# Performance work log

Hardware: AMD Instinct MI355X
Metric: run time of the kernel (lower is better)

Reference implementation:

```python
import jax, jax.numpy as jnp
import numpy as np

B = 1024        # probe batch
Q = 65536       # queue_size (number of identities in momentum queue)
D = 512         # feat_dim
MARGIN = 0.4
SCALE = 32.0
HARD_NEG = 10   # min(max(int(Q*0.0002), 3), 10)


def setup_inputs() -> dict:
    key = jax.random.key(0)
    k1, k2, k3, k4 = jax.random.split(key, 4)
    p = jax.random.normal(k1, (B, D), dtype=jnp.float32)
    p = p / jnp.linalg.norm(p, axis=1, keepdims=True)
    queue = jax.random.uniform(k2, (2, Q, D), dtype=jnp.float32)
    queue = queue / jnp.linalg.norm(queue, axis=2, keepdims=True)  # F.normalize(queue, dim=2)
    label = jax.random.randint(k3, (B,), 0, Q)
    label = jnp.where(jnp.arange(B) % 4 == 0, -1, label)
    # binary mask buffer marking queue slots whose second copy is active
    mask = (jax.random.uniform(k4, (Q, 1)) < 0.1).astype(jnp.float32)
    return {"p": p, "queue": queue, "mask": mask, "label": label}


def _add_margin_am(cos_theta, label):
    # cos_theta: [B, Q], label: [B] with -1 marking outliers
    pos_mask = label != -1                                  # [B]
    safe_label = jnp.where(pos_mask, label, 0)
    onehot = jax.nn.one_hot(safe_label, cos_theta.shape[1], dtype=cos_theta.dtype)
    # AM-softmax: subtract margin at the ground-truth logit, then scale + CE
    logits = (cos_theta - MARGIN * onehot) * SCALE          # [B, Q]
    log_z = jax.nn.logsumexp(logits, axis=1)                # [B]
    gt = jnp.take_along_axis(cos_theta, safe_label[:, None], axis=1)[:, 0]
    ce = log_z - (gt - MARGIN) * SCALE                      # per-row cross entropy
    n_pos = jnp.sum(pos_mask)
    cls_loss = jnp.where(
        n_pos > 0,
        jnp.sum(jnp.where(pos_mask, ce, 0.0)) / jnp.maximum(n_pos, 1),
        0.0,
    )
    # hard-negative mining over outlier rows: top-k (replaces torch argsort+gather)
    top_vals, _ = jax.lax.top_k(cos_theta, HARD_NEG)        # [B, HARD_NEG]
    hard = jnp.clip(top_vals, 0.0)
    neg_per_row = jnp.mean(hard, axis=1)                    # [B]
    n_neg = jnp.sum(~pos_mask)
    neg_loss = jnp.where(
        n_neg > 0,
        jnp.sum(jnp.where(~pos_mask, neg_per_row, 0.0)) / jnp.maximum(n_neg, 1),
        0.0,
    )
    return cls_loss + neg_loss


def reference(p, queue, mask, label):
    # cos_theta1 = F.linear(p, queue[0])
    cos1 = jnp.einsum('bd,qd->bq', p, queue[0])
    # weight = mask * queue[1] + (1 - mask) * queue[0]  (computed under no_grad in torch)
    weight = mask * queue[1] + (1.0 - mask) * queue[0]
    cos2 = jnp.einsum('bd,qd->bq', p, weight)
    loss = _add_margin_am(cos1, label) + _add_margin_am(cos2, label)
    return loss
```

## Files before the change

kernel.cpp:

```cpp
#include <hip/hip_runtime.h>
#include <stdint.h>

#define B_ 1024
#define Q_ 65536
#define D_ 512
#define MT 128
#define NT 128
#define BK 64
#define NSPLIT 64
#define NCHUNK (Q_ / NSPLIT)
#define NTILES (NCHUNK / NT)
#define KITERS (D_ / BK)

#define WS_ACC  0
#define WS_LSE  1024
#define WS_TOPK (WS_LSE + 2 * B_ * NSPLIT * 2 * 4)
#define WS_PBF  (8u * 1024u * 1024u)
#define WS_QBF  (16u * 1024u * 1024u)

#define SA_OFF 0
#define SB0_OFF 16384
#define SB1_OFF 32768
#define EPI_STRIDE 264
#define EPI1_OFF 33792
#define SMEM_BYTES 67584

typedef __attribute__((ext_vector_type(8))) short short8;
typedef __attribute__((ext_vector_type(4))) short short4v;
typedef __attribute__((ext_vector_type(4))) float f32x4;

__device__ __forceinline__ unsigned short f2bf(float x) {
  union { float f; uint32_t u; } v; v.f = x;
  uint32_t r = v.u + 0x7fffu + ((v.u >> 16) & 1u);
  return (unsigned short)(r >> 16);
}

__device__ __forceinline__ float bf2f(short u) {
  union { uint32_t i; float f; } v;
  v.i = ((uint32_t)(unsigned short)u) << 16;
  return v.f;
}

__device__ __forceinline__ void async16(void* lds, const void* g) {
  void* gg = (void*)g;
  __builtin_amdgcn_global_load_lds(
      (__attribute__((address_space(1))) unsigned int*)gg,
      (__attribute__((address_space(3))) unsigned int*)lds,
      16, 0, 0);
}

__device__ __forceinline__ void lse_bf_row(const unsigned char* rowp,
                                           float& M, float& Z) {
  float tmax = -1e30f;
#pragma unroll
  for (int c = 0; c < 32; ++c) {
    short4v v = *(const short4v*)(rowp + c * 8);
    tmax = fmaxf(tmax, fmaxf(fmaxf(bf2f(v.x), bf2f(v.y)),
                             fmaxf(bf2f(v.z), bf2f(v.w))));
  }
  float Mn = fmaxf(M, tmax * 32.0f);
  float fac = __expf(M - Mn);
  float s = 0.0f;
#pragma unroll
  for (int c = 0; c < 32; ++c) {
    short4v v = *(const short4v*)(rowp + c * 8);
    s += __expf(fmaf(bf2f(v.x), 32.0f, -Mn));
    s += __expf(fmaf(bf2f(v.y), 32.0f, -Mn));
    s += __expf(fmaf(bf2f(v.z), 32.0f, -Mn));
    s += __expf(fmaf(bf2f(v.w), 32.0f, -Mn));
  }
  Z = fmaf(Z, fac, s);
  M = Mn;
}

__device__ __forceinline__ void tkins(float v,
    float& t0, float& t1, float& t2, float& t3, float& t4,
    float& t5, float& t6, float& t7, float& t8, float& t9) {
  if (v > t9) {
    t9 = (v > t8) ? t8 : v;
    t8 = (v > t8) ? ((v > t7) ? t7 : v) : t8;
    t7 = (v > t7) ? ((v > t6) ? t6 : v) : t7;
    t6 = (v > t6) ? ((v > t5) ? t5 : v) : t6;
    t5 = (v > t5) ? ((v > t4) ? t4 : v) : t5;
    t4 = (v > t4) ? ((v > t3) ? t3 : v) : t4;
    t3 = (v > t3) ? ((v > t2) ? t2 : v) : t3;
    t2 = (v > t2) ? ((v > t1) ? t1 : v) : t2;
    t1 = (v > t1) ? ((v > t0) ? t0 : v) : t1;
    t0 = (v > t0) ? v : t0;
  }
}

#define TK10(v, base) tkins((v), rs[(base)+0], rs[(base)+1], rs[(base)+2], rs[(base)+3], \
    rs[(base)+4], rs[(base)+5], rs[(base)+6], rs[(base)+7], rs[(base)+8], rs[(base)+9])

__global__ void cvt_bf16_kernel(const float* __restrict__ src,
                                unsigned short* __restrict__ dst, int n8) {
  int i = blockIdx.x * blockDim.x + threadIdx.x;
  int stride = gridDim.x * blockDim.x;
  for (; i < n8; i += stride) {
    const float4* s = (const float4*)src + (size_t)2 * i;
    float4 a = s[0], b = s[1];
    short8 o;
    o[0] = (short)f2bf(a.x); o[1] = (short)f2bf(a.y);
    o[2] = (short)f2bf(a.z); o[3] = (short)f2bf(a.w);
    o[4] = (short)f2bf(b.x); o[5] = (short)f2bf(b.y);
    o[6] = (short)f2bf(b.z); o[7] = (short)f2bf(b.w);
    *(short8*)(dst + (size_t)i * 8) = o;
  }
}

__global__ __launch_bounds__(256, 2) void fused_gemm_partial(
    const unsigned short* __restrict__ pbf, const unsigned short* __restrict__ qbf,
    const float* __restrict__ maskp, const int* __restrict__ label,
    char* __restrict__ ws) {
  __shared__ __align__(16) unsigned char smem[SMEM_BYTES];
  __shared__ float maskbuf[NT];
  __shared__ int olist[MT];
  __shared__ int sh_ocount;

  float* tlbuf = (float*)smem;

  const int tid = threadIdx.x;
  const int mblk = blockIdx.x;
  const int split = blockIdx.y;
  const int lane = tid & 63;
  const int wv = tid >> 6;
  const int wr = wv >> 1;
  const int wc = wv & 1;
  const int lr = lane & 15;
  const int lg = lane >> 4;

  if (tid == 0) sh_ocount = 0;
  __syncthreads();
  if (tid < MT) {
    if (label[mblk * MT + tid] == -1) {
      int k = atomicAdd(&sh_ocount, 1);
      olist[k] = tid;
    }
  }
  __syncthreads();
  const int noc = sh_ocount;
  int rowloc = -1;
  int sub = 0;
  if (tid >= 128) {
    int task = (tid - 128) >> 2;
    sub = (tid - 128) & 3;
    if (task < noc) rowloc = olist[task];
  }

  const int srow = lane >> 3;
  const int sc16 = (lane & 7) ^ srow;
  const size_t g_lane_off = (size_t)srow * D_ + sc16 * 8;

  float rs[20];
#pragma unroll
  for (int i = 0; i < 20; ++i) rs[i] = -1e30f;
  if (tid < MT) { rs[1] = 0.0f; rs[3] = 0.0f; }

  for (int nt = 0; nt < NTILES; ++nt) {
    const int nbase = split * NCHUNK + nt * NT;
    if (tid < NT) maskbuf[tid] = maskp[nbase + tid];

    f32x4 acc0[4][4], acc1[4][4];
#pragma unroll
    for (int i = 0; i < 4; ++i)
#pragma unroll
      for (int j = 0; j < 4; ++j) {
        f32x4 z = {0.0f, 0.0f, 0.0f, 0.0f};
        acc0[i][j] = z;
        acc1[i][j] = z;
      }

    for (int kk = 0; kk < KITERS; ++kk) {
      const size_t kcol = (size_t)kk * BK;
#pragma unroll
      for (int t = 0; t < 4; ++t) {
        const int slot = wv * 4 + t;
        const size_t rbase = (size_t)slot * 8;
        async16(smem + SA_OFF + slot * 1024,
                pbf + ((size_t)mblk * MT + rbase) * D_ + kcol + g_lane_off);
        async16(smem + SB0_OFF + slot * 1024,
                qbf + ((size_t)nbase + rbase) * D_ + kcol + g_lane_off);
        async16(smem + SB1_OFF + slot * 1024,
                qbf + ((size_t)Q_ + nbase + rbase) * D_ + kcol + g_lane_off);
      }
      __syncthreads();

#pragma unroll
      for (int s = 0; s < 2; ++s) {
        const int xs = ((s * 4 + lg) ^ (lr & 7)) * 16;
        short8 af[4], bf0[4], bf1[4];
#pragma unroll
        for (int i = 0; i < 4; ++i)
          af[i] = *(const short8*)(smem + SA_OFF + (wr * 64 + i * 16 + lr) * 128 + xs);
#pragma unroll
        for (int j = 0; j < 4; ++j) {
          bf0[j] = *(const short8*)(smem + SB0_OFF + (wc * 64 + j * 16 + lr) * 128 + xs);
          bf1[j] = *(const short8*)(smem + SB1_OFF + (wc * 64 + j * 16 + lr) * 128 + xs);
        }
#pragma unroll
        for (int i = 0; i < 4; ++i)
#pragma unroll
          for (int j = 0; j < 4; ++j) {
            acc0[i][j] = __builtin_amdgcn_mfma_f32_16x16x32_bf16(af[i], bf0[j], acc0[i][j], 0, 0, 0);
            acc1[i][j] = __builtin_amdgcn_mfma_f32_16x16x32_bf16(af[i], bf1[j], acc1[i][j], 0, 0, 0);
          }
      }
      __syncthreads();
    }

    float mcol[4];
#pragma unroll
    for (int j = 0; j < 4; ++j) mcol[j] = maskbuf[wc * 64 + j * 16 + lr];
#pragma unroll
    for (int i = 0; i < 4; ++i)
#pragma unroll
      for (int j = 0; j < 4; ++j)
#pragma unroll
        for (int k = 0; k < 4; ++k) {
          const int r = wr * 64 + i * 16 + lg * 4 + k;
          const int c = wc * 64 + j * 16 + lr;
          float g0 = acc0[i][j][k], g1 = acc1[i][j][k];
          *(unsigned short*)(smem + r * EPI_STRIDE + c * 2) = f2bf(g0);
          *(unsigned short*)(smem + EPI1_OFF + r * EPI_STRIDE + c * 2) =
              f2bf(fmaf(mcol[j], g1 - g0, g0));
        }
    __syncthreads();

    if (tid < MT) {
      lse_bf_row(smem + tid * EPI_STRIDE, rs[0], rs[1]);
      lse_bf_row(smem + EPI1_OFF + tid * EPI_STRIDE, rs[2], rs[3]);
    } else if (rowloc >= 0) {
      const unsigned char* b0 = smem + rowloc * EPI_STRIDE + sub * 64;
#pragma unroll
      for (int c = 0; c < 8; ++c) {
        short4v v = *(const short4v*)(b0 + c * 8);
        TK10(bf2f(v.x), 0); TK10(bf2f(v.y), 0);
        TK10(bf2f(v.z), 0); TK10(bf2f(v.w), 0);
      }
      const unsigned char* b1 = b0 + EPI1_OFF;
#pragma unroll
      for (int c = 0; c < 8; ++c) {
        short4v v = *(const short4v*)(b1 + c * 8);
        TK10(bf2f(v.x), 10); TK10(bf2f(v.y), 10);
        TK10(bf2f(v.z), 10); TK10(bf2f(v.w), 10);
      }
    }
    __syncthreads();
  }

  if (tid < MT) {
    int grow = mblk * MT + tid;
    float2* lseo = (float2*)(ws + WS_LSE);
    lseo[((size_t)0 * B_ + grow) * NSPLIT + split] = make_float2(rs[0], rs[1]);
    lseo[((size_t)1 * B_ + grow) * NSPLIT + split] = make_float2(rs[2], rs[3]);
  }
  if (tid >= 128) {
    float* dst = &tlbuf[(tid - 128) * 20];
#pragma unroll
    for (int i = 0; i < 20; ++i) dst[i] = rs[i];
  }
  __syncthreads();
  if (tid < 64) {
    int l = tid & 1, o = tid >> 1;
    if (o < noc) {
      float m0 = -1e30f, m1 = -1e30f, m2 = -1e30f, m3 = -1e30f, m4 = -1e30f;
      float m5 = -1e30f, m6 = -1e30f, m7 = -1e30f, m8 = -1e30f, m9 = -1e30f;
#pragma unroll
      for (int s = 0; s < 4; ++s)
#pragma unroll
        for (int i = 0; i < 10; ++i)
          tkins(tlbuf[(o * 4 + s) * 20 + l * 10 + i], m0, m1, m2, m3, m4, m5, m6, m7, m8, m9);
      int grow = mblk * MT + olist[o];
      float* dst = (float*)(ws + WS_TOPK) + ((size_t)(l * B_ + grow) * NSPLIT + (size_t)split) * 10;
      dst[0] = m0; dst[1] = m1; dst[2] = m2; dst[3] = m3; dst[4] = m4;
      dst[5] = m5; dst[6] = m6; dst[7] = m7; dst[8] = m8; dst[9] = m9;
    }
  }
}

__global__ void finalize_rows(
    const float* __restrict__ p, const float* __restrict__ queue,
    const float* __restrict__ maskp, const int* __restrict__ label,
    char* __restrict__ ws) {
  const int row = blockIdx.x;
  const int l = threadIdx.x >> 6;
  const int lane = threadIdx.x & 63;
  const int lab = label[row];
  float* wsf = (float*)ws;
  int* wsi = (int*)ws;

  if (lab != -1) {
    const float2* lsep = (const float2*)(ws + WS_LSE);
    float2 mz = lsep[((size_t)l * B_ + row) * NSPLIT + lane];
    float M = mz.x;
    float Mx = M;
#pragma unroll
    for (int o = 1; o < 64; o <<= 1) Mx = fmaxf(Mx, __shfl_xor(Mx, o, 64));
    float z = mz.y * __expf(M - Mx);
#pragma unroll
    for (int o = 1; o < 64; o <<= 1) z += __shfl_xor(z, o, 64);

    const float* prow = p + (size_t)row * D_;
    const float* q0r = queue + (size_t)lab * D_;
    const float* q1r = queue + ((size_t)Q_ + (size_t)lab) * D_;
    int c = lane * 8;
    float4 a0 = *(const float4*)(prow + c);
    float4 a1 = *(const float4*)(prow + c + 4);
    float4 b0 = *(const float4*)(q0r + c);
    float4 b1 = *(const float4*)(q0r + c + 4);
    float d0 = a0.x * b0.x + a0.y * b0.y + a0.z * b0.z + a0.w * b0.w
             + a1.x * b1.x + a1.y * b1.y + a1.z * b1.z + a1.w * b1.w;
    float d1 = 0.0f;
    if (l == 1) {
      float4 c0 = *(const float4*)(q1r + c);
      float4 c1 = *(const float4*)(q1r + c + 4);
      d1 = a0.x * c0.x + a0.y * c0.y + a0.z * c0.z + a0.w * c0.w
         + a1.x * c1.x + a1.y * c1.y + a1.z * c1.z + a1.w * c1.w;
    }
#pragma unroll
    for (int o = 1; o < 64; o <<= 1) {
      d0 += __shfl_xor(d0, o, 64);
      d1 += __shfl_xor(d1, o, 64);
    }
    float gt;
    if (l == 0) gt = d0;
    else { float m = maskp[lab]; gt = fmaf(m, d1 - d0, d0); }

    if (lane == 0) {
      float t1 = __expf(fmaf(gt, 32.0f, -Mx));
      float t2 = __expf(fmaf(gt - 0.4f, 32.0f, -Mx));
      float Zc = z - t1 + t2;
      float ce = Mx + __logf(Zc) - (gt - 0.4f) * 32.0f;
      atomicAdd(&wsf[0], ce);
      if (l == 0) atomicAdd(&wsi[2], 1);
    }
  } else {
    const float* tp = (const float*)(ws + WS_TOPK) +
                      ((size_t)(l * B_ + row) * NSPLIT + (size_t)lane) * 10;
    float t0 = tp[0], t1 = tp[1], t2 = tp[2], t3 = tp[3], t4 = tp[4];
    float t5 = tp[5], t6 = tp[6], t7 = tp[7], t8 = tp[8], t9 = tp[9];
    float ssum = 0.0f;
#pragma unroll
    for (int r10 = 0; r10 < 10; ++r10) {
      float v = t0;
      int idx = lane;
#pragma unroll
      for (int o = 1; o < 64; o <<= 1) {
        float ov = __shfl_xor(v, o, 64);
        int oi = __shfl_xor(idx, o, 64);
        bool take = (ov > v) || (ov == v && oi < idx);
        v = take ? ov : v;
        idx = take ? oi : idx;
      }
      ssum += fmaxf(v, 0.0f);
      if (idx == lane) {
        t0 = t1; t1 = t2; t2 = t3; t3 = t4; t4 = t5;
        t5 = t6; t6 = t7; t7 = t8; t8 = t9; t9 = -1e30f;
      }
    }
    if (lane == 0) {
      atomicAdd(&wsf[1], ssum * 0.1f);
      if (l == 0) atomicAdd(&wsi[3], 1);
    }
  }
}

__global__ void finalize_scalar(const char* __restrict__ ws, float* __restrict__ out) {
  const float* wsf = (const float*)ws;
  const int* wsi = (const int*)ws;
  float loss = 0.0f;
  if (wsi[2] > 0) loss += wsf[0] / (float)wsi[2];
  if (wsi[3] > 0) loss += wsf[1] / (float)wsi[3];
  out[0] = loss;
}

extern "C" void kernel_launch(void* const* d_in, const int* in_sizes, int n_in,
                              void* d_out, int out_size, void* d_ws, size_t ws_size,
                              hipStream_t stream) {
  const float* p     = (const float*)d_in[0];
  const float* queue = (const float*)d_in[1];
  const float* maskp = (const float*)d_in[2];
  const int*   label = (const int*)d_in[3];
  float* out = (float*)d_out;
  char* ws = (char*)d_ws;

  unsigned short* pbf = (unsigned short*)(ws + WS_PBF);
  unsigned short* qbf = (unsigned short*)(ws + WS_QBF);

  hipMemsetAsync(ws, 0, 16, stream);

  cvt_bf16_kernel<<<4096, 256, 0, stream>>>(queue, qbf, (2 * Q_ * D_) / 8);
  cvt_bf16_kernel<<<256, 256, 0, stream>>>(p, pbf, (B_ * D_) / 8);

  dim3 g1(B_ / MT, NSPLIT);
  fused_gemm_partial<<<g1, 256, 0, stream>>>(pbf, qbf, maskp, label, ws);
  finalize_rows<<<B_, 128, 0, stream>>>(p, queue, maskp, label, ws);
  finalize_scalar<<<1, 1, 0, stream>>>(ws, out);
}
```

Before: 638.9 us.

## Precompute mixed weight matrix in conversion pass and split GEMM per logit set

The conversion kernel now blends queue[0] and queue[1] by the mask into a separate bf16 weight matrix, and reads queue[1] only for rows whose mask is set. Each GEMM block therefore computes one logit set, against either queue0 or the blended weight. This drops the per-element mask blend in the epilogue, halves the accumulator registers and LDS per block, and raises occupancy to three blocks per CU. The split count doubles and the grid is reordered, which increases the partial results the finalize kernel must merge. Numerics change slightly because the blend now happens in fp32 before the bf16 rounding.

```diff
diff --git a/kernel.cpp b/kernel.cpp
--- a/kernel.cpp
+++ b/kernel.cpp
@@ -7,7 +7,7 @@
 #define MT 128
 #define NT 128
 #define BK 64
-#define NSPLIT 64
+#define NSPLIT 128
 #define NCHUNK (Q_ / NSPLIT)
 #define NTILES (NCHUNK / NT)
 #define KITERS (D_ / BK)
@@ -15,15 +15,14 @@
 #define WS_ACC  0
 #define WS_LSE  1024
 #define WS_TOPK (WS_LSE + 2 * B_ * NSPLIT * 2 * 4)
-#define WS_PBF  (8u * 1024u * 1024u)
-#define WS_QBF  (16u * 1024u * 1024u)
+#define WS_PBF  (13u * 1024u * 1024u)
+#define WS_QBF0 (14u * 1024u * 1024u)
+#define WS_WBF  (78u * 1024u * 1024u)
 
 #define SA_OFF 0
-#define SB0_OFF 16384
-#define SB1_OFF 32768
+#define SB_OFF 16384
 #define EPI_STRIDE 264
-#define EPI1_OFF 33792
-#define SMEM_BYTES 67584
+#define SMEM_BYTES 33792
 
 typedef __attribute__((ext_vector_type(8))) short short8;
 typedef __attribute__((ext_vector_type(4))) short short4v;
@@ -90,8 +89,39 @@
   }
 }
 
-#define TK10(v, base) tkins((v), rs[(base)+0], rs[(base)+1], rs[(base)+2], rs[(base)+3], \
-    rs[(base)+4], rs[(base)+5], rs[(base)+6], rs[(base)+7], rs[(base)+8], rs[(base)+9])
+#define TK10(v) tkins((v), rs[0], rs[1], rs[2], rs[3], rs[4], rs[5], rs[6], rs[7], rs[8], rs[9])
+
+__global__ void cvt_queue_kernel(const float* __restrict__ q,
+                                 const float* __restrict__ mask,
+                                 unsigned short* __restrict__ qbf0,
+                                 unsigned short* __restrict__ wbf) {
+  const int row = blockIdx.x * 4 + (threadIdx.x >> 6);
+  const int lane = threadIdx.x & 63;
+  const float* q0r = q + (size_t)row * D_ + lane * 8;
+  float4 a = ((const float4*)q0r)[0];
+  float4 b = ((const float4*)q0r)[1];
+  short8 o;
+  o[0] = (short)f2bf(a.x); o[1] = (short)f2bf(a.y);
+  o[2] = (short)f2bf(a.z); o[3] = (short)f2bf(a.w);
+  o[4] = (short)f2bf(b.x); o[5] = (short)f2bf(b.y);
+  o[6] = (short)f2bf(b.z); o[7] = (short)f2bf(b.w);
+  *(short8*)(qbf0 + (size_t)row * D_ + lane * 8) = o;
+  float m = mask[row];
+  if (m != 0.0f) {
+    const float* q1r = q0r + (size_t)Q_ * D_;
+    float4 c = ((const float4*)q1r)[0];
+    float4 d = ((const float4*)q1r)[1];
+    a.x = fmaf(m, c.x - a.x, a.x); a.y = fmaf(m, c.y - a.y, a.y);
+    a.z = fmaf(m, c.z - a.z, a.z); a.w = fmaf(m, c.w - a.w, a.w);
+    b.x = fmaf(m, d.x - b.x, b.x); b.y = fmaf(m, d.y - b.y, b.y);
+    b.z = fmaf(m, d.z - b.z, b.z); b.w = fmaf(m, d.w - b.w, b.w);
+    o[0] = (short)f2bf(a.x); o[1] = (short)f2bf(a.y);
+    o[2] = (short)f2bf(a.z); o[3] = (short)f2bf(a.w);
+    o[4] = (short)f2bf(b.x); o[5] = (short)f2bf(b.y);
+    o[6] = (short)f2bf(b.z); o[7] = (short)f2bf(b.w);
+  }
+  *(short8*)(wbf + (size_t)row * D_ + lane * 8) = o;
+}
 
 __global__ void cvt_bf16_kernel(const float* __restrict__ src,
                                 unsigned short* __restrict__ dst, int n8) {
@@ -109,20 +139,22 @@
   }
 }
 
-__global__ __launch_bounds__(256, 2) void fused_gemm_partial(
-    const unsigned short* __restrict__ pbf, const unsigned short* __restrict__ qbf,
-    const float* __restrict__ maskp, const int* __restrict__ label,
+__global__ __launch_bounds__(256, 3) void fused_gemm_partial(
+    const unsigned short* __restrict__ pbf,
+    const unsigned short* __restrict__ qbf0,
+    const unsigned short* __restrict__ wbf,
+    const int* __restrict__ label,
     char* __restrict__ ws) {
   __shared__ __align__(16) unsigned char smem[SMEM_BYTES];
-  __shared__ float maskbuf[NT];
   __shared__ int olist[MT];
   __shared__ int sh_ocount;
-
   float* tlbuf = (float*)smem;
 
   const int tid = threadIdx.x;
-  const int mblk = blockIdx.x;
-  const int split = blockIdx.y;
+  const int split = blockIdx.x;
+  const int mblk = blockIdx.y >> 1;
+  const int which = blockIdx.y & 1;
+  const unsigned short* bsrc = which ? wbf : qbf0;
   const int lane = tid & 63;
   const int wv = tid >> 6;
   const int wr = wv >> 1;
@@ -152,23 +184,21 @@
   const int sc16 = (lane & 7) ^ srow;
   const size_t g_lane_off = (size_t)srow * D_ + sc16 * 8;
 
-  float rs[20];
-#pragma unroll
-  for (int i = 0; i < 20; ++i) rs[i] = -1e30f;
-  if (tid < MT) { rs[1] = 0.0f; rs[3] = 0.0f; }
+  float rs[10];
+#pragma unroll
+  for (int i = 0; i < 10; ++i) rs[i] = -1e30f;
+  if (tid < MT) rs[1] = 0.0f;
 
   for (int nt = 0; nt < NTILES; ++nt) {
     const int nbase = split * NCHUNK + nt * NT;
-    if (tid < NT) maskbuf[tid] = maskp[nbase + tid];
-
-    f32x4 acc0[4][4], acc1[4][4];
+
+    f32x4 acc[4][4];
 #pragma unroll
     for (int i = 0; i < 4; ++i)
 #pragma unroll
       for (int j = 0; j < 4; ++j) {
         f32x4 z = {0.0f, 0.0f, 0.0f, 0.0f};
-        acc0[i][j] = z;
-        acc1[i][j] = z;
+        acc[i][j] = z;
       }
 
     for (int kk = 0; kk < KITERS; ++kk) {
@@ -179,39 +209,30 @@
         const size_t rbase = (size_t)slot * 8;
         async16(smem + SA_OFF + slot * 1024,
                 pbf + ((size_t)mblk * MT + rbase) * D_ + kcol + g_lane_off);
-        async16(smem + SB0_OFF + slot * 1024,
-                qbf + ((size_t)nbase + rbase) * D_ + kcol + g_lane_off);
-        async16(smem + SB1_OFF + slot * 1024,
-                qbf + ((size_t)Q_ + nbase + rbase) * D_ + kcol + g_lane_off);
+        async16(smem + SB_OFF + slot * 1024,
+                bsrc + ((size_t)nbase + rbase) * D_ + kcol + g_lane_off);
       }
       __syncthreads();
 
 #pragma unroll
       for (int s = 0; s < 2; ++s) {
         const int xs = ((s * 4 + lg) ^ (lr & 7)) * 16;
-        short8 af[4], bf0[4], bf1[4];
+        short8 af[4], bf[4];
 #pragma unroll
         for (int i = 0; i < 4; ++i)
           af[i] = *(const short8*)(smem + SA_OFF + (wr * 64 + i * 16 + lr) * 128 + xs);
 #pragma unroll
-        for (int j = 0; j < 4; ++j) {
-          bf0[j] = *(const short8*)(smem + SB0_OFF + (wc * 64 + j * 16 + lr) * 128 + xs);
-          bf1[j] = *(const short8*)(smem + SB1_OFF + (wc * 64 + j * 16 + lr) * 128 + xs);
-        }
+        for (int j = 0; j < 4; ++j)
+          bf[j] = *(const short8*)(smem + SB_OFF + (wc * 64 + j * 16 + lr) * 128 + xs);
 #pragma unroll
         for (int i = 0; i < 4; ++i)
 #pragma unroll
-          for (int j = 0; j < 4; ++j) {
-            acc0[i][j] = __builtin_amdgcn_mfma_f32_16x16x32_bf16(af[i], bf0[j], acc0[i][j], 0, 0, 0);
-            acc1[i][j] = __builtin_amdgcn_mfma_f32_16x16x32_bf16(af[i], bf1[j], acc1[i][j], 0, 0, 0);
-          }
+          for (int j = 0; j < 4; ++j)
+            acc[i][j] = __builtin_amdgcn_mfma_f32_16x16x32_bf16(af[i], bf[j], acc[i][j], 0, 0, 0);
       }
       __syncthreads();
     }
 
-    float mcol[4];
-#pragma unroll
-    for (int j = 0; j < 4; ++j) mcol[j] = maskbuf[wc * 64 + j * 16 + lr];
 #pragma unroll
     for (int i = 0; i < 4; ++i)
 #pragma unroll
@@ -220,30 +241,17 @@
         for (int k = 0; k < 4; ++k) {
           const int r = wr * 64 + i * 16 + lg * 4 + k;
           const int c = wc * 64 + j * 16 + lr;
-          float g0 = acc0[i][j][k], g1 = acc1[i][j][k];
-          *(unsigned short*)(smem + r * EPI_STRIDE + c * 2) = f2bf(g0);
-          *(unsigned short*)(smem + EPI1_OFF + r * EPI_STRIDE + c * 2) =
-              f2bf(fmaf(mcol[j], g1 - g0, g0));
+          *(unsigned short*)(smem + r * EPI_STRIDE + c * 2) = f2bf(acc[i][j][k]);
         }
     __syncthreads();
-
     if (tid < MT) {
       lse_bf_row(smem + tid * EPI_STRIDE, rs[0], rs[1]);
-      lse_bf_row(smem + EPI1_OFF + tid * EPI_STRIDE, rs[2], rs[3]);
     } else if (rowloc >= 0) {
       const unsigned char* b0 = smem + rowloc * EPI_STRIDE + sub * 64;
 #pragma unroll
       for (int c = 0; c < 8; ++c) {
         short4v v = *(const short4v*)(b0 + c * 8);
-        TK10(bf2f(v.x), 0); TK10(bf2f(v.y), 0);
-        TK10(bf2f(v.z), 0); TK10(bf2f(v.w), 0);
-      }
-      const unsigned char* b1 = b0 + EPI1_OFF;
-#pragma unroll
-      for (int c = 0; c < 8; ++c) {
-        short4v v = *(const short4v*)(b1 + c * 8);
-        TK10(bf2f(v.x), 10); TK10(bf2f(v.y), 10);
-        TK10(bf2f(v.z), 10); TK10(bf2f(v.w), 10);
+        TK10(bf2f(v.x)); TK10(bf2f(v.y)); TK10(bf2f(v.z)); TK10(bf2f(v.w));
       }
     }
     __syncthreads();
@@ -252,30 +260,27 @@
   if (tid < MT) {
     int grow = mblk * MT + tid;
     float2* lseo = (float2*)(ws + WS_LSE);
-    lseo[((size_t)0 * B_ + grow) * NSPLIT + split] = make_float2(rs[0], rs[1]);
-    lseo[((size_t)1 * B_ + grow) * NSPLIT + split] = make_float2(rs[2], rs[3]);
+    lseo[((size_t)which * B_ + grow) * NSPLIT + split] = make_float2(rs[0], rs[1]);
   }
   if (tid >= 128) {
-    float* dst = &tlbuf[(tid - 128) * 20];
-#pragma unroll
-    for (int i = 0; i < 20; ++i) dst[i] = rs[i];
+    float* dst = &tlbuf[(tid - 128) * 10];
+#pragma unroll
+    for (int i = 0; i < 10; ++i) dst[i] = rs[i];
   }
   __syncthreads();
-  if (tid < 64) {
-    int l = tid & 1, o = tid >> 1;
-    if (o < noc) {
-      float m0 = -1e30f, m1 = -1e30f, m2 = -1e30f, m3 = -1e30f, m4 = -1e30f;
-      float m5 = -1e30f, m6 = -1e30f, m7 = -1e30f, m8 = -1e30f, m9 = -1e30f;
-#pragma unroll
-      for (int s = 0; s < 4; ++s)
-#pragma unroll
-        for (int i = 0; i < 10; ++i)
-          tkins(tlbuf[(o * 4 + s) * 20 + l * 10 + i], m0, m1, m2, m3, m4, m5, m6, m7, m8, m9);
-      int grow = mblk * MT + olist[o];
-      float* dst = (float*)(ws + WS_TOPK) + ((size_t)(l * B_ + grow) * NSPLIT + (size_t)split) * 10;
-      dst[0] = m0; dst[1] = m1; dst[2] = m2; dst[3] = m3; dst[4] = m4;
-      dst[5] = m5; dst[6] = m6; dst[7] = m7; dst[8] = m8; dst[9] = m9;
-    }
+  if (tid < 32 && tid < noc) {
+    float m0 = -1e30f, m1 = -1e30f, m2 = -1e30f, m3 = -1e30f, m4 = -1e30f;
+    float m5 = -1e30f, m6 = -1e30f, m7 = -1e30f, m8 = -1e30f, m9 = -1e30f;
+#pragma unroll
+    for (int s = 0; s < 4; ++s)
+#pragma unroll
+      for (int i = 0; i < 10; ++i)
+        tkins(tlbuf[(tid * 4 + s) * 10 + i], m0, m1, m2, m3, m4, m5, m6, m7, m8, m9);
+    int grow = mblk * MT + olist[tid];
+    float* dst = (float*)(ws + WS_TOPK) +
+                 ((size_t)which * B_ + grow) * NSPLIT * 10 + (size_t)split * 10;
+    dst[0] = m0; dst[1] = m1; dst[2] = m2; dst[3] = m3; dst[4] = m4;
+    dst[5] = m5; dst[6] = m6; dst[7] = m7; dst[8] = m8; dst[9] = m9;
   }
 }
 
@@ -291,13 +296,15 @@
   int* wsi = (int*)ws;
 
   if (lab != -1) {
-    const float2* lsep = (const float2*)(ws + WS_LSE);
-    float2 mz = lsep[((size_t)l * B_ + row) * NSPLIT + lane];
-    float M = mz.x;
+    const float2* lsep = (const float2*)(ws + WS_LSE) + ((size_t)l * B_ + row) * NSPLIT;
+    float2 a = lsep[lane];
+    float2 b = lsep[lane + 64];
+    float M = fmaxf(a.x, b.x);
+    float z = a.y * __expf(a.x - M) + b.y * __expf(b.x - M);
     float Mx = M;
 #pragma unroll
     for (int o = 1; o < 64; o <<= 1) Mx = fmaxf(Mx, __shfl_xor(Mx, o, 64));
-    float z = mz.y * __expf(M - Mx);
+    z *= __expf(M - Mx);
 #pragma unroll
     for (int o = 1; o < 64; o <<= 1) z += __shfl_xor(z, o, 64);
 
@@ -336,10 +343,14 @@
       if (l == 0) atomicAdd(&wsi[2], 1);
     }
   } else {
-    const float* tp = (const float*)(ws + WS_TOPK) +
-                      ((size_t)(l * B_ + row) * NSPLIT + (size_t)lane) * 10;
-    float t0 = tp[0], t1 = tp[1], t2 = tp[2], t3 = tp[3], t4 = tp[4];
-    float t5 = tp[5], t6 = tp[6], t7 = tp[7], t8 = tp[8], t9 = tp[9];
+    const float* tp = (const float*)(ws + WS_TOPK) + ((size_t)l * B_ + row) * NSPLIT * 10;
+    const float* pa = tp + (size_t)lane * 10;
+    const float* pb = tp + (size_t)(lane + 64) * 10;
+    float t0 = pa[0], t1 = pa[1], t2 = pa[2], t3 = pa[3], t4 = pa[4];
+    float t5 = pa[5], t6 = pa[6], t7 = pa[7], t8 = pa[8], t9 = pa[9];
+#pragma unroll
+    for (int i = 0; i < 10; ++i)
+      tkins(pb[i], t0, t1, t2, t3, t4, t5, t6, t7, t8, t9);
     float ssum = 0.0f;
 #pragma unroll
     for (int r10 = 0; r10 < 10; ++r10) {
@@ -385,16 +396,17 @@
   float* out = (float*)d_out;
   char* ws = (char*)d_ws;
 
-  unsigned short* pbf = (unsigned short*)(ws + WS_PBF);
-  unsigned short* qbf = (unsigned short*)(ws + WS_QBF);
+  unsigned short* pbf  = (unsigned short*)(ws + WS_PBF);
+  unsigned short* qbf0 = (unsigned short*)(ws + WS_QBF0);
+  unsigned short* wbf  = (unsigned short*)(ws + WS_WBF);
 
   hipMemsetAsync(ws, 0, 16, stream);
 
-  cvt_bf16_kernel<<<4096, 256, 0, stream>>>(queue, qbf, (2 * Q_ * D_) / 8);
+  cvt_queue_kernel<<<Q_ / 4, 256, 0, stream>>>(queue, maskp, qbf0, wbf);
   cvt_bf16_kernel<<<256, 256, 0, stream>>>(p, pbf, (B_ * D_) / 8);
 
-  dim3 g1(B_ / MT, NSPLIT);
-  fused_gemm_partial<<<g1, 256, 0, stream>>>(pbf, qbf, maskp, label, ws);
+  dim3 g1(NSPLIT, 16);
+  fused_gemm_partial<<<g1, 256, 0, stream>>>(pbf, qbf0, wbf, label, ws);
   finalize_rows<<<B_, 128, 0, stream>>>(p, queue, maskp, label, ws);
   finalize_scalar<<<1, 1, 0, stream>>>(ws, out);
 }
```

Result: slower. 718.4 us (+12.4%).
